# Kernel tuning notes

Measured on AMD Instinct MI355X. Metric: run time of the kernel, lower is better.

## Reference

```python
import jax, jax.numpy as jnp
import numpy as np
import math

B, S, HID = 2, 2048, 2048
NUM_HEADS = 32
NUM_GROUPS = 4
NUM_KV = NUM_HEADS // NUM_GROUPS  # 8 KV heads
HEAD_DIM = HID // NUM_HEADS       # 64


def setup_inputs() -> dict:
    key = jax.random.key(0)
    ks = jax.random.split(key, 9)
    def lin(kw, fan_in, fan_out):
        # torch Linear init: U(-1/sqrt(fan_in), 1/sqrt(fan_in)); stored as [in, out]
        bound = 1.0 / math.sqrt(fan_in)
        return jax.random.uniform(kw, (fan_in, fan_out), jnp.float32, -bound, bound)
    x = jax.random.normal(ks[0], (B, S, HID), jnp.float32)
    # causal mask: True = masked (upper triangle), broadcast over batch
    causal = jnp.triu(jnp.ones((S, S), dtype=bool), k=1)
    mask = jnp.broadcast_to(causal, (B, S, S))
    bound_h = 1.0 / math.sqrt(HID)
    return {
        "x": x,
        "mask": mask,
        "Wq": lin(ks[1], HID, NUM_HEADS * HEAD_DIM),
        "bq": jax.random.uniform(ks[2], (NUM_HEADS * HEAD_DIM,), jnp.float32, -bound_h, bound_h),
        "Wk": lin(ks[3], HID, NUM_KV * HEAD_DIM),
        "bk": jax.random.uniform(ks[4], (NUM_KV * HEAD_DIM,), jnp.float32, -bound_h, bound_h),
        "Wv": lin(ks[5], HID, NUM_KV * HEAD_DIM),
        "bv": jax.random.uniform(ks[6], (NUM_KV * HEAD_DIM,), jnp.float32, -bound_h, bound_h),
        "Wo": lin(ks[7], HID, HID),
        "bo": jax.random.uniform(ks[8], (HID,), jnp.float32, -bound_h, bound_h),
    }


def reference(x, mask, Wq, bq, Wk, bk, Wv, bv, Wo, bo):
    Bq, Sq, _ = x.shape
    q = x @ Wq + bq  # [B,S,Hq*D]
    k = x @ Wk + bk  # [B,S,Hkv*D]
    v = x @ Wv + bv
    # group Q heads by their KV head: repeat_interleave(G, dim=1) on KV means
    # q head h uses kv head h // G, i.e. q reshaped [B, Hkv, G, S, D]
    q = q.reshape(Bq, Sq, NUM_KV, NUM_GROUPS, HEAD_DIM).transpose(0, 2, 3, 1, 4)  # [B,Hkv,G,S,D]
    k = k.reshape(Bq, Sq, NUM_KV, HEAD_DIM).transpose(0, 2, 1, 3)                 # [B,Hkv,S,D]
    v = v.reshape(Bq, Sq, NUM_KV, HEAD_DIM).transpose(0, 2, 1, 3)                 # [B,Hkv,S,D]
    scale = 1.0 / math.sqrt(HEAD_DIM)
    scores = jnp.einsum('bkgsd,bktd->bkgst', q, k) * scale  # [B,Hkv,G,S,S]
    scores = jnp.where(mask[:, None, None, :, :], -jnp.inf, scores)
    attn = jax.nn.softmax(scores, axis=-1)
    out = jnp.einsum('bkgst,bktd->bkgsd', attn, v)          # [B,Hkv,G,S,D]
    out = out.transpose(0, 3, 1, 2, 4).reshape(Bq, Sq, HID)  # [B,S,Hq*D]
    return out @ Wo + bo
```

## Files before the change

kernel.cpp:

```cpp
#include <hip/hip_runtime.h>

typedef unsigned short u16;
typedef __attribute__((ext_vector_type(8))) short s16x8;
typedef __attribute__((ext_vector_type(4))) short s16x4;
typedef __attribute__((ext_vector_type(8))) unsigned short u16x8;
typedef __attribute__((ext_vector_type(4))) unsigned short u16x4;
typedef __attribute__((ext_vector_type(4))) float f32x4;

#define B_ 2
#define S_ 2048
#define HID_ 2048
#define NH_ 32
#define NKV_ 8
#define HD_ 64
#define M_ (B_ * S_)
#define NQKV_ 3072

__device__ __forceinline__ u16 bf16rne(float f) {
    union { float f; unsigned u; } x; x.f = f;
    unsigned u = x.u;
    u += 0x7fffu + ((u >> 16) & 1u);
    return (u16)(u >> 16);
}
__device__ __forceinline__ float bf16tof(u16 h) {
    union { unsigned u; float f; } x; x.u = ((unsigned)h) << 16;
    return x.f;
}
__device__ __forceinline__ f32x4 vmax4(f32x4 a, f32x4 b) {
    f32x4 r;
    r[0] = fmaxf(a[0], b[0]); r[1] = fmaxf(a[1], b[1]);
    r[2] = fmaxf(a[2], b[2]); r[3] = fmaxf(a[3], b[3]);
    return r;
}
__device__ __forceinline__ f32x4 mfma16x16x16_bf16(s16x4 a, s16x4 b, f32x4 c) {
#if __has_builtin(__builtin_amdgcn_mfma_f32_16x16x16bf16_1k)
    return __builtin_amdgcn_mfma_f32_16x16x16bf16_1k(a, b, c, 0, 0, 0);
#else
    f32x4 d = c;
    asm volatile("v_mfma_f32_16x16x16_bf16 %0, %1, %2, %0" : "+v"(d) : "v"(a), "v"(b));
    return d;
#endif
}

__device__ __forceinline__ void gload16(const void* g, void* l) {
    __builtin_amdgcn_global_load_lds(
        (const __attribute__((address_space(1))) unsigned int*)g,
        (__attribute__((address_space(3))) unsigned int*)l, 16, 0, 0);
}

__global__ __launch_bounds__(256) void convert_x_kernel(const float* __restrict__ src,
                                                        u16* __restrict__ dst, int n4) {
    int i = blockIdx.x * 256 + threadIdx.x;
    if (i >= n4) return;
    f32x4 v = *(const f32x4*)(src + (size_t)i * 4);
    u16x4 o;
    o[0] = bf16rne(v[0]); o[1] = bf16rne(v[1]); o[2] = bf16rne(v[2]); o[3] = bf16rne(v[3]);
    *(u16x4*)(dst + (size_t)i * 4) = o;
}

__global__ void pack_bias_kernel(const float* bq, const float* bk, const float* bv,
                                 float* __restrict__ dst) {
    int i = blockIdx.x * 256 + threadIdx.x;
    if (i >= NQKV_) return;
    float v;
    if (i < 2048) v = bq[i];
    else if (i < 2560) v = bk[i - 2048];
    else v = bv[i - 2560];
    dst[i] = v;
}

__global__ __launch_bounds__(256) void transpose_w_all_kernel(
    const float* __restrict__ Wq, const float* __restrict__ Wk,
    const float* __restrict__ Wv, const float* __restrict__ Wo,
    u16* __restrict__ wqkvT, u16* __restrict__ woT) {
    __shared__ float tile[32][33];
    int z = blockIdx.z;
    const float* src; u16* dst; int N;
    if (z == 0)      { src = Wq; dst = wqkvT;                          N = 2048; }
    else if (z == 1) { src = Wk; dst = wqkvT + (size_t)2048 * 2048;    N = 512;  }
    else if (z == 2) { src = Wv; dst = wqkvT + (size_t)2560 * 2048;    N = 512;  }
    else             { src = Wo; dst = woT;                            N = 2048; }
    int n0 = blockIdx.x * 32;
    if (n0 >= N) return;
    int k0 = blockIdx.y * 32;
    int tx = threadIdx.x;
    int ty = threadIdx.y;
    for (int i = 0; i < 32; i += 8)
        tile[ty + i][tx] = src[(size_t)(k0 + ty + i) * N + n0 + tx];
    __syncthreads();
    for (int i = 0; i < 32; i += 8)
        dst[(size_t)(n0 + ty + i) * 2048 + k0 + tx] = bf16rne(tile[tx][ty + i]);
}

template <bool OUT_BF16, bool FUSE_VT>
__global__ __launch_bounds__(256) void gemm_bt_kernel(const u16* __restrict__ A,
                                                      const u16* __restrict__ Bt,
                                                      const float* __restrict__ bias,
                                                      void* __restrict__ Cout,
                                                      u16* __restrict__ vTp,
                                                      int M, int N, int K) {
    __shared__ u16 As[128][64];
    __shared__ u16 Bs[128][64];
    int nwg = (int)(gridDim.x * gridDim.y);
    int bid = (int)(blockIdx.y * gridDim.x + blockIdx.x);
    int swz = (bid & 7) * (nwg >> 3) + (bid >> 3);
    int bn = (swz % (int)gridDim.x) * 128;
    int bm = (swz / (int)gridDim.x) * 128;
    int tid = threadIdx.x;
    int lane = tid & 63, wid = tid >> 6;
    int wr = wid >> 1, wc = wid & 1;
    int lr = lane & 15, lg = lane >> 4;
    f32x4 acc[4][4] = {};

    int srow_l = lane >> 3;
    int schunk = (lane & 7) ^ srow_l;
    int scol = schunk * 8;

    for (int k0 = 0; k0 < K; k0 += 64) {
        __syncthreads();
#pragma unroll
        for (int c = 0; c < 4; c++) {
            int row = c * 32 + wid * 8;
            gload16(A + (size_t)(bm + row + srow_l) * K + k0 + scol, &As[row][0]);
            gload16(Bt + (size_t)(bn + row + srow_l) * K + k0 + scol, &Bs[row][0]);
        }
        asm volatile("s_waitcnt vmcnt(0)" ::: "memory");
        __syncthreads();
#pragma unroll
        for (int kk = 0; kk < 2; kk++) {
            s16x8 a[4], b[4];
#pragma unroll
            for (int mi = 0; mi < 4; mi++) {
                int row = wr * 64 + mi * 16 + lr;
                int cc = ((kk << 2) + lg) ^ (lr & 7);
                a[mi] = *(const s16x8*)&As[row][cc << 3];
            }
#pragma unroll
            for (int ni = 0; ni < 4; ni++) {
                int row = wc * 64 + ni * 16 + lr;
                int cc = ((kk << 2) + lg) ^ (lr & 7);
                b[ni] = *(const s16x8*)&Bs[row][cc << 3];
            }
#pragma unroll
            for (int mi = 0; mi < 4; mi++)
#pragma unroll
                for (int ni = 0; ni < 4; ni++)
                    acc[mi][ni] = __builtin_amdgcn_mfma_f32_16x16x32_bf16(a[mi], b[ni], acc[mi][ni], 0, 0, 0);
        }
    }

#pragma unroll
    for (int mi = 0; mi < 4; mi++)
#pragma unroll
        for (int ni = 0; ni < 4; ni++) {
            int col = bn + wc * 64 + ni * 16 + lr;
            float bsv = bias ? bias[col] : 0.0f;
            int row0 = bm + wr * 64 + mi * 16 + lg * 4;
            if (FUSE_VT && col >= 2560) {
                int kvd = col - 2560;
                int bq_ = row0 >> 11;
                int s0 = row0 & 2047;
                u16x4 w;
#pragma unroll
                for (int r = 0; r < 4; r++) w[r] = bf16rne(acc[mi][ni][r] + bsv);
                *(u16x4*)(vTp + (size_t)(bq_ * 8 * 64 + kvd) * 2048 + s0) = w;
            } else {
#pragma unroll
                for (int r = 0; r < 4; r++) {
                    float v = acc[mi][ni][r] + bsv;
                    if (OUT_BF16)
                        ((u16*)Cout)[(size_t)(row0 + r) * N + col] = bf16rne(v);
                    else
                        ((float*)Cout)[(size_t)(row0 + r) * N + col] = v;
                }
            }
        }
}

__global__ __launch_bounds__(512) void attn_kernel(const u16* __restrict__ qkv,
                                                   const u16* __restrict__ vT,
                                                   u16* __restrict__ attn_out) {
    int bx = blockIdx.x;
    int bkv = blockIdx.y;
    int b = bkv >> 3, kvh = bkv & 7;
    int tid = threadIdx.x;
    int lane = tid & 63, wid = tid >> 6;
    int lr = lane & 15, lg = lane >> 4;
    int h = kvh * 4 + (wid >> 1);
    int sub = wid & 1;

    __shared__ u16 Ks[2][64][72];
    __shared__ u16 Vs[2][64][72];

    const u16* Kbase = qkv + (size_t)(b * S_) * NQKV_ + 2048 + kvh * 64;
    const u16* Vbase = vT + (size_t)(b * 8 + kvh) * 64 * S_;

    int srow = tid >> 3;
    int scol = (tid & 7) * 8;

#pragma unroll 1
    for (int phase = 0; phase < 2; phase++) {
        int qt = phase ? (63 - bx) : bx;
        int qrow0 = qt * 32 + sub * 16;
        int nt = qt / 2 + 1;

        s16x8 qf[2];
        {
            const u16* qr = qkv + (size_t)(b * S_ + qrow0 + lr) * NQKV_ + h * 64;
#pragma unroll
            for (int db = 0; db < 2; db++) {
                u16x8 u = *(const u16x8*)(qr + db * 32 + lg * 8);
                s16x8 s;
#pragma unroll
                for (int j = 0; j < 8; j++) s[j] = (short)bf16rne(bf16tof(u[j]) * 0.18033688f);
                qf[db] = s;
            }
        }

        f32x4 O[4] = {};
        float m_i = -1e30f, l_i = 0.0f;

        {
            u16x8 k0v = *(const u16x8*)(Kbase + (size_t)srow * NQKV_ + scol);
            u16x8 v0v = *(const u16x8*)(Vbase + (size_t)srow * S_ + scol);
            *(u16x8*)&Ks[0][srow][scol] = k0v;
            *(u16x8*)&Vs[0][srow][scol] = v0v;
        }
        __syncthreads();

        int cb = 0;
        for (int t = 0; t < nt; t++) {
            int kv0 = t * 64;
            bool notlast = (t + 1 < nt);
            u16x8 kn, vn;
            if (notlast) {
                kn = *(const u16x8*)(Kbase + (size_t)(kv0 + 64 + srow) * NQKV_ + scol);
                vn = *(const u16x8*)(Vbase + (size_t)srow * S_ + kv0 + 64 + scol);
            }

            f32x4 Sc[4] = {};
            __builtin_amdgcn_s_setprio(1);
#pragma unroll
            for (int t4 = 0; t4 < 4; t4++) {
#pragma unroll
                for (int db = 0; db < 2; db++) {
                    s16x8 kf = *(const s16x8*)&Ks[cb][t4 * 16 + lr][db * 32 + lg * 8];
                    Sc[t4] = __builtin_amdgcn_mfma_f32_16x16x32_bf16(kf, qf[db], Sc[t4], 0, 0, 0);
                }
            }
            __builtin_amdgcn_s_setprio(0);
            if (t == nt - 1) {
                int qr = qrow0 + lr;
#pragma unroll
                for (int t4 = 0; t4 < 4; t4++)
#pragma unroll
                    for (int r = 0; r < 4; r++) {
                        int kvi = kv0 + t4 * 16 + lg * 4 + r;
                        Sc[t4][r] = (kvi <= qr) ? Sc[t4][r] : -1e30f;
                    }
            }
            f32x4 mm = vmax4(vmax4(Sc[0], Sc[1]), vmax4(Sc[2], Sc[3]));
            float mx = fmaxf(fmaxf(mm[0], mm[1]), fmaxf(mm[2], mm[3]));
            mx = fmaxf(mx, __shfl_xor(mx, 16));
            mx = fmaxf(mx, __shfl_xor(mx, 32));
            float newm = fmaxf(m_i, mx);
            float alpha = exp2f(m_i - newm);
            m_i = newm;
            f32x4 p4[4];
#pragma unroll
            for (int t4 = 0; t4 < 4; t4++)
#pragma unroll
                for (int r = 0; r < 4; r++)
                    p4[t4][r] = exp2f(Sc[t4][r] - newm);
            f32x4 ss = (p4[0] + p4[1]) + (p4[2] + p4[3]);
            float rs = (ss[0] + ss[1]) + (ss[2] + ss[3]);
            rs += __shfl_xor(rs, 16);
            rs += __shfl_xor(rs, 32);
            l_i = l_i * alpha + rs;
#pragma unroll
            for (int dt = 0; dt < 4; dt++)
#pragma unroll
                for (int r = 0; r < 4; r++) O[dt][r] *= alpha;
            s16x4 pa[4];
#pragma unroll
            for (int t4 = 0; t4 < 4; t4++) {
                u16x4 w;
#pragma unroll
                for (int r = 0; r < 4; r++) w[r] = bf16rne(p4[t4][r]);
                union { u16x4 u; s16x4 s; } uu; uu.u = w;
                pa[t4] = uu.s;
            }
            __builtin_amdgcn_s_setprio(1);
#pragma unroll
            for (int t4 = 0; t4 < 4; t4++) {
#pragma unroll
                for (int dt = 0; dt < 4; dt++) {
                    s16x4 va = *(const s16x4*)&Vs[cb][dt * 16 + lr][t4 * 16 + lg * 4];
                    O[dt] = mfma16x16x16_bf16(va, pa[t4], O[dt]);
                }
            }
            __builtin_amdgcn_s_setprio(0);
            if (notlast) {
                *(u16x8*)&Ks[cb ^ 1][srow][scol] = kn;
                *(u16x8*)&Vs[cb ^ 1][srow][scol] = vn;
            }
            __syncthreads();
            cb ^= 1;
        }

        float il = 1.0f / l_i;
        u16* orow = attn_out + (size_t)(b * S_ + qrow0 + lr) * HID_ + h * 64 + lg * 4;
#pragma unroll
        for (int dt = 0; dt < 4; dt++) {
            u16x4 w;
#pragma unroll
            for (int r = 0; r < 4; r++) w[r] = bf16rne(O[dt][r] * il);
            *(u16x4*)(orow + dt * 16) = w;
        }
    }
}

extern "C" void kernel_launch(void* const* d_in, const int* in_sizes, int n_in,
                              void* d_out, int out_size, void* d_ws, size_t ws_size,
                              hipStream_t stream) {
    const float* x  = (const float*)d_in[0];
    const float* Wq = (const float*)d_in[2];
    const float* bq = (const float*)d_in[3];
    const float* Wk = (const float*)d_in[4];
    const float* bk = (const float*)d_in[5];
    const float* Wv = (const float*)d_in[6];
    const float* bv = (const float*)d_in[7];
    const float* Wo = (const float*)d_in[8];
    const float* bo = (const float*)d_in[9];
    float* out = (float*)d_out;

    char* ws = (char*)d_ws;
    u16* xb     = (u16*)(ws);
    u16* wqkvT  = (u16*)(ws + 16777216);
    u16* woT    = (u16*)(ws + 29360128);
    u16* qkv    = (u16*)(ws + 37748736);
    u16* vT     = (u16*)(ws + 62914560);
    u16* attnO  = (u16*)(ws + 67108864);
    float* biasQ = (float*)(ws + 83886080);

    {
        int n4 = (M_ * HID_) / 4;
        convert_x_kernel<<<(n4 + 255) / 256, 256, 0, stream>>>(x, xb, n4);
    }
    pack_bias_kernel<<<(NQKV_ + 255) / 256, 256, 0, stream>>>(bq, bk, bv, biasQ);
    transpose_w_all_kernel<<<dim3(64, 64, 4), dim3(32, 8), 0, stream>>>(
        Wq, Wk, Wv, Wo, wqkvT, woT);
    gemm_bt_kernel<true, true><<<dim3(NQKV_ / 128, M_ / 128), 256, 0, stream>>>(
        xb, wqkvT, biasQ, qkv, vT, M_, NQKV_, HID_);
    attn_kernel<<<dim3(32, B_ * NKV_), 512, 0, stream>>>(qkv, vT, attnO);
    gemm_bt_kernel<false, false><<<dim3(HID_ / 128, M_ / 128), 256, 0, stream>>>(
        attnO, woT, bo, out, nullptr, M_, HID_, HID_);
}
```

Before: 223.0 us.

## Split long causal attention rows across two blocks with split-KV combine

Attention now launches two blocks per (bx, batch, kv-head). One block handles the short query tile plus the first part of the long tile's KV range. The other handles the rest of the long tile's KV range, with partial O, m and l written to workspace. A new combine kernel merges the two partials for the second half of the sequence. This doubles the grid from 512 to 1024 blocks to improve CU occupancy and balance, at the cost of an extra kernel launch, extra partial-result traffic, and bf16 rounding of the unnormalized partials. The partial buffers reuse the xb/weight workspace region, which is assumed dead by then.

```diff
diff --git a/kernel.cpp b/kernel.cpp
--- a/kernel.cpp
+++ b/kernel.cpp
@@ -177,33 +177,23 @@
         }
 }
 
-__global__ __launch_bounds__(512) void attn_kernel(const u16* __restrict__ qkv,
-                                                   const u16* __restrict__ vT,
-                                                   u16* __restrict__ attn_out) {
-    int bx = blockIdx.x;
-    int bkv = blockIdx.y;
-    int b = bkv >> 3, kvh = bkv & 7;
-    int tid = threadIdx.x;
-    int lane = tid & 63, wid = tid >> 6;
-    int lr = lane & 15, lg = lane >> 4;
-    int h = kvh * 4 + (wid >> 1);
-    int sub = wid & 1;
-
-    __shared__ u16 Ks[2][64][72];
-    __shared__ u16 Vs[2][64][72];
+__device__ __forceinline__ void attn_run(
+    const u16* __restrict__ qkv, const u16* __restrict__ vT,
+    u16* __restrict__ attn_out, u16* __restrict__ partO, float* __restrict__ ml,
+    int b, int kvh, int h, int sub, int tid, int lr, int lg,
+    int qt, int t0, int t1, int mode,
+    u16 Ks[2][64][72], u16 Vs[2][64][72]) {
+    int qrow0 = qt * 32 + sub * 16;
+    int Tm1 = qt >> 1;
+    f32x4 O[4] = {};
+    float m_i = -1e30f, l_i = 0.0f;
 
     const u16* Kbase = qkv + (size_t)(b * S_) * NQKV_ + 2048 + kvh * 64;
     const u16* Vbase = vT + (size_t)(b * 8 + kvh) * 64 * S_;
-
     int srow = tid >> 3;
     int scol = (tid & 7) * 8;
 
-#pragma unroll 1
-    for (int phase = 0; phase < 2; phase++) {
-        int qt = phase ? (63 - bx) : bx;
-        int qrow0 = qt * 32 + sub * 16;
-        int nt = qt / 2 + 1;
-
+    if (t0 < t1) {
         s16x8 qf[2];
         {
             const u16* qr = qkv + (size_t)(b * S_ + qrow0 + lr) * NQKV_ + h * 64;
@@ -216,28 +206,23 @@
                 qf[db] = s;
             }
         }
-
-        f32x4 O[4] = {};
-        float m_i = -1e30f, l_i = 0.0f;
-
         {
-            u16x8 k0v = *(const u16x8*)(Kbase + (size_t)srow * NQKV_ + scol);
-            u16x8 v0v = *(const u16x8*)(Vbase + (size_t)srow * S_ + scol);
+            u16x8 k0v = *(const u16x8*)(Kbase + (size_t)(t0 * 64 + srow) * NQKV_ + scol);
+            u16x8 v0v = *(const u16x8*)(Vbase + (size_t)srow * S_ + t0 * 64 + scol);
             *(u16x8*)&Ks[0][srow][scol] = k0v;
             *(u16x8*)&Vs[0][srow][scol] = v0v;
         }
         __syncthreads();
 
         int cb = 0;
-        for (int t = 0; t < nt; t++) {
+        for (int t = t0; t < t1; t++) {
             int kv0 = t * 64;
-            bool notlast = (t + 1 < nt);
+            bool notlast = (t + 1 < t1);
             u16x8 kn, vn;
             if (notlast) {
                 kn = *(const u16x8*)(Kbase + (size_t)(kv0 + 64 + srow) * NQKV_ + scol);
                 vn = *(const u16x8*)(Vbase + (size_t)srow * S_ + kv0 + 64 + scol);
             }
-
             f32x4 Sc[4] = {};
             __builtin_amdgcn_s_setprio(1);
 #pragma unroll
@@ -249,7 +234,7 @@
                 }
             }
             __builtin_amdgcn_s_setprio(0);
-            if (t == nt - 1) {
+            if (t == Tm1) {
                 int qr = qrow0 + lr;
 #pragma unroll
                 for (int t4 = 0; t4 < 4; t4++)
@@ -307,7 +292,9 @@
             __syncthreads();
             cb ^= 1;
         }
-
+    }
+
+    if (mode == 0) {
         float il = 1.0f / l_i;
         u16* orow = attn_out + (size_t)(b * S_ + qrow0 + lr) * HID_ + h * 64 + lg * 4;
 #pragma unroll
@@ -317,7 +304,80 @@
             for (int r = 0; r < 4; r++) w[r] = bf16rne(O[dt][r] * il);
             *(u16x4*)(orow + dt * 16) = w;
         }
+    } else {
+        int pr = (b * 32 + h) * 1024 + (qrow0 + lr - 1024);
+#pragma unroll
+        for (int dt = 0; dt < 4; dt++) {
+            u16x4 w;
+#pragma unroll
+            for (int r = 0; r < 4; r++) w[r] = bf16rne(O[dt][r]);
+            *(u16x4*)(partO + (size_t)pr * 64 + dt * 16 + lg * 4) = w;
+        }
+        if (lg == 0) {
+            ml[(size_t)pr * 4 + (mode - 1) * 2]     = m_i;
+            ml[(size_t)pr * 4 + (mode - 1) * 2 + 1] = l_i;
+        }
     }
+}
+
+__global__ __launch_bounds__(512) void attn_kernel(const u16* __restrict__ qkv,
+                                                   const u16* __restrict__ vT,
+                                                   u16* __restrict__ attn_out,
+                                                   u16* __restrict__ partO0,
+                                                   u16* __restrict__ partO1,
+                                                   float* __restrict__ ml) {
+    int bx = blockIdx.x;
+    int bkv = blockIdx.y;
+    int hf = blockIdx.z;
+    int b = bkv >> 3, kvh = bkv & 7;
+    int tid = threadIdx.x;
+    int lane = tid & 63, wid = tid >> 6;
+    int lr = lane & 15, lg = lane >> 4;
+    int h = kvh * 4 + (wid >> 1);
+    int sub = wid & 1;
+
+    __shared__ u16 Ks[2][64][72];
+    __shared__ u16 Vs[2][64][72];
+
+    int Ta = (bx >> 1) + 1;
+    int qh = 63 - bx;
+    int Th = (qh >> 1) + 1;
+    int p = (Th - Ta) >> 1;
+
+    if (hf == 0) {
+        attn_run(qkv, vT, attn_out, partO0, ml, b, kvh, h, sub, tid, lr, lg,
+                 bx, 0, Ta, 0, Ks, Vs);
+        attn_run(qkv, vT, attn_out, partO0, ml, b, kvh, h, sub, tid, lr, lg,
+                 qh, 0, p, 1, Ks, Vs);
+    } else {
+        attn_run(qkv, vT, attn_out, partO1, ml, b, kvh, h, sub, tid, lr, lg,
+                 qh, p, Th, 2, Ks, Vs);
+    }
+}
+
+__global__ __launch_bounds__(256) void combine_kernel(const u16* __restrict__ partO0,
+                                                      const u16* __restrict__ partO1,
+                                                      const float* __restrict__ ml,
+                                                      u16* __restrict__ attn_out) {
+    int tid = threadIdx.x;
+    int rowInBlk = tid >> 3;
+    int seg = tid & 7;
+    int pr = blockIdx.x * 32 + rowInBlk;
+    int b = pr >> 15;
+    int h = (pr >> 10) & 31;
+    int s = (pr & 1023) + 1024;
+    float m0 = ml[(size_t)pr * 4 + 0], l0 = ml[(size_t)pr * 4 + 1];
+    float m1 = ml[(size_t)pr * 4 + 2], l1 = ml[(size_t)pr * 4 + 3];
+    float mx = fmaxf(m0, m1);
+    float a0 = exp2f(m0 - mx), a1 = exp2f(m1 - mx);
+    float rden = 1.0f / (a0 * l0 + a1 * l1);
+    u16x8 o0 = *(const u16x8*)(partO0 + (size_t)pr * 64 + seg * 8);
+    u16x8 o1 = *(const u16x8*)(partO1 + (size_t)pr * 64 + seg * 8);
+    u16x8 w;
+#pragma unroll
+    for (int j = 0; j < 8; j++)
+        w[j] = bf16rne((a0 * bf16tof(o0[j]) + a1 * bf16tof(o1[j])) * rden);
+    *(u16x8*)(attn_out + (size_t)(b * S_ + s) * HID_ + h * 64 + seg * 8) = w;
 }
 
 extern "C" void kernel_launch(void* const* d_in, const int* in_sizes, int n_in,
@@ -342,6 +402,9 @@
     u16* vT     = (u16*)(ws + 62914560);
     u16* attnO  = (u16*)(ws + 67108864);
     float* biasQ = (float*)(ws + 83886080);
+    u16* partO0 = (u16*)(ws);
+    u16* partO1 = (u16*)(ws + 8388608);
+    float* mlBuf = (float*)(ws + 16777216);
 
     {
         int n4 = (M_ * HID_) / 4;
@@ -352,7 +415,9 @@
         Wq, Wk, Wv, Wo, wqkvT, woT);
     gemm_bt_kernel<true, true><<<dim3(NQKV_ / 128, M_ / 128), 256, 0, stream>>>(
         xb, wqkvT, biasQ, qkv, vT, M_, NQKV_, HID_);
-    attn_kernel<<<dim3(32, B_ * NKV_), 512, 0, stream>>>(qkv, vT, attnO);
+    attn_kernel<<<dim3(32, B_ * NKV_, 2), 512, 0, stream>>>(
+        qkv, vT, attnO, partO0, partO1, mlBuf);
+    combine_kernel<<<2048, 256, 0, stream>>>(partO0, partO1, mlBuf, attnO);
     gemm_bt_kernel<false, false><<<dim3(HID_ / 128, M_ / 128), 256, 0, stream>>>(
         attnO, woT, bo, out, nullptr, M_, HID_, HID_);
 }
```

Measured after the change: 233.3 us. 1.05x slower.
